# Kernel optimization log

Hardware: AMD Instinct MI355X
Metric: run time of the kernel (lower is better)

Reference implementation:

```python
import jax, jax.numpy as jnp
import numpy as np

NUM_NODES = 100_000
NUM_EDGES = 20_000
NNZ = 1_000_000


def setup_inputs() -> dict:
    key = jax.random.key(0)
    ks = jax.random.split(key, 8)
    d_in, d_hid, d_out = 128, 256, 40
    return {
        "x": jax.random.normal(ks[0], (NUM_NODES, d_in), dtype=jnp.float32),
        "node_idx": jax.random.randint(ks[1], (NNZ,), 0, NUM_NODES, dtype=jnp.int32),
        "edge_idx": jax.random.randint(ks[2], (NNZ,), 0, NUM_EDGES, dtype=jnp.int32),
        "W1": jax.random.normal(ks[3], (d_in, d_hid), dtype=jnp.float32) * (1.0 / np.sqrt(d_in)),
        "b1": jnp.zeros((d_hid,), dtype=jnp.float32),
        "W2": jax.random.normal(ks[4], (d_hid, d_hid), dtype=jnp.float32) * (1.0 / np.sqrt(d_hid)),
        "b2": jnp.zeros((d_hid,), dtype=jnp.float32),
        "W3": jax.random.normal(ks[5], (d_hid, d_out), dtype=jnp.float32) * (1.0 / np.sqrt(d_hid)),
        "b3": jnp.zeros((d_out,), dtype=jnp.float32),
    }


def _degree_norms(node_idx, edge_idx):
    # D = per-node incidence count (hyperedge_weight = ones); B = per-hyperedge node count
    ones = jnp.ones((node_idx.shape[0],), dtype=jnp.float32)
    D = jax.ops.segment_sum(ones, node_idx, num_segments=NUM_NODES)
    B = jax.ops.segment_sum(ones, edge_idx, num_segments=NUM_EDGES)
    Dinv = jnp.where(D > 0, 1.0 / D, 0.0)  # 1/D with inf -> 0, per PyG
    Binv = jnp.where(B > 0, 1.0 / B, 0.0)
    return Dinv, Binv


def _hconv(x, W, b, node_idx, edge_idx, Dinv, Binv):
    # PyG HypergraphConv (use_attention=False): X' = D^{-1} H B^{-1} H^T X W + b
    x = x @ W                                                            # [N, F]
    m = jax.ops.segment_sum(x[node_idx], edge_idx, num_segments=NUM_EDGES)  # H^T X W -> [E, F]
    m = Binv[:, None] * m
    out = jax.ops.segment_sum(m[edge_idx], node_idx, num_segments=NUM_NODES)  # [N, F]
    return Dinv[:, None] * out + b


def reference(x, node_idx, edge_idx, W1, b1, W2, b2, W3, b3):
    Dinv, Binv = _degree_norms(node_idx, edge_idx)
    # conv layers 0..L-2: conv -> ELU -> dropout (eval mode: identity)
    h = jax.nn.elu(_hconv(x, W1, b1, node_idx, edge_idx, Dinv, Binv))
    h = jax.nn.elu(_hconv(h, W2, b2, node_idx, edge_idx, Dinv, Binv))
    # final conv, no activation
    return _hconv(h, W3, b3, node_idx, edge_idx, Dinv, Binv)
```

## Files before the change

kernel.cpp:

```cpp
#include <hip/hip_runtime.h>
#include <cstdint>
#include <cstddef>

constexpr int N_NODES = 100000;
constexpr int N_EDGES = 20000;
constexpr int NNZ     = 1000000;
constexpr int NPAD    = 100096;
constexpr int EPAD    = 20096;

typedef __attribute__((ext_vector_type(8))) __bf16 bf16x8;
typedef __attribute__((ext_vector_type(4))) float f32x4;

__device__ __forceinline__ unsigned short bf16_rne(float v) {
  unsigned u = __builtin_bit_cast(unsigned, v);
  return (unsigned short)((u + 0x7FFFu + ((u >> 16) & 1u)) >> 16);
}
__device__ __forceinline__ void split2(float v, unsigned short& h, unsigned short& l) {
  unsigned u = __builtin_bit_cast(unsigned, v);
  unsigned hb = (u + 0x7FFFu + ((u >> 16) & 1u)) & 0xFFFF0000u;
  h = (unsigned short)(hb >> 16);
  float lo = v - __builtin_bit_cast(float, hb);
  l = bf16_rne(lo);
}
__device__ __forceinline__ float elu_f(float x) { return x > 0.f ? x : expm1f(x); }

__device__ __forceinline__ void gload_lds16(const void* g, void* l) {
  __builtin_amdgcn_global_load_lds(
      (const __attribute__((address_space(1))) unsigned int*)(uintptr_t)g,
      (__attribute__((address_space(3))) unsigned int*)(uintptr_t)l, 16, 0, 0);
}

__global__ void count_kernel(const int* __restrict__ ni, const int* __restrict__ ei,
                             int* __restrict__ dcnt, int* __restrict__ bcnt) {
  int i = blockIdx.x * blockDim.x + threadIdx.x;
  if (i < NNZ) {
    atomicAdd(&dcnt[ni[i]], 1);
    atomicAdd(&bcnt[ei[i]], 1);
  }
}

__global__ void invert2_kernel(const int* __restrict__ dcnt, const int* __restrict__ bcnt,
                               float* __restrict__ dinv, float* __restrict__ binv) {
  int i = blockIdx.x * blockDim.x + threadIdx.x;
  if (i < N_NODES) {
    int c = dcnt[i];
    dinv[i] = c > 0 ? 1.0f / (float)c : 0.0f;
  }
  if (i < N_EDGES) {
    int c = bcnt[i];
    binv[i] = c > 0 ? 1.0f / (float)c : 0.0f;
  }
}

__device__ __forceinline__ void scan_block_body(const int* __restrict__ cnt, int n,
                                                int* __restrict__ out,
                                                int* __restrict__ partials, int bid) {
  __shared__ int buf[256];
  int tid = threadIdx.x;
  int i = bid * 256 + tid;
  int v = (i < n) ? cnt[i] : 0;
  buf[tid] = v;
  __syncthreads();
  for (int o = 1; o < 256; o <<= 1) {
    int t = (tid >= o) ? buf[tid - o] : 0;
    __syncthreads();
    buf[tid] += t;
    __syncthreads();
  }
  if (i < n) out[i] = buf[tid] - v;
  if (tid == 255) partials[bid] = buf[tid];
}

__global__ void scan_block2(const int* __restrict__ c1, int n1, int* __restrict__ o1,
                            int* __restrict__ p1, int nb1,
                            const int* __restrict__ c2, int n2, int* __restrict__ o2,
                            int* __restrict__ p2) {
  if ((int)blockIdx.x < nb1) scan_block_body(c1, n1, o1, p1, blockIdx.x);
  else scan_block_body(c2, n2, o2, p2, blockIdx.x - nb1);
}

__device__ __forceinline__ void scan_partials_body(int* __restrict__ partials, int nb,
                                                   int* __restrict__ total_out) {
  __shared__ int buf[1024];
  int tid = threadIdx.x;
  int v = (tid < nb) ? partials[tid] : 0;
  buf[tid] = v;
  __syncthreads();
  for (int o = 1; o < 1024; o <<= 1) {
    int t = (tid >= o) ? buf[tid - o] : 0;
    __syncthreads();
    buf[tid] += t;
    __syncthreads();
  }
  if (tid < nb) partials[tid] = buf[tid] - v;
  if (tid == 1023) *total_out = buf[1023];
}

__global__ void scan_partials2(int* __restrict__ p1, int nb1, int* __restrict__ t1,
                               int* __restrict__ p2, int nb2, int* __restrict__ t2) {
  if (blockIdx.x == 0) scan_partials_body(p1, nb1, t1);
  else scan_partials_body(p2, nb2, t2);
}

__global__ void scan_add2(int* __restrict__ o1, int n1, const int* __restrict__ p1, int nb1,
                          int* __restrict__ o2, int n2, const int* __restrict__ p2) {
  if ((int)blockIdx.x < nb1) {
    int i = blockIdx.x * 256 + threadIdx.x;
    if (i < n1) o1[i] += p1[blockIdx.x];
  } else {
    int b = blockIdx.x - nb1;
    int i = b * 256 + threadIdx.x;
    if (i < n2) o2[i] += p2[b];
  }
}

__global__ void fill_kernel(const int* __restrict__ ni, const int* __restrict__ ei,
                            const int* __restrict__ noff, const int* __restrict__ eoff,
                            int* __restrict__ ncur, int* __restrict__ ecur,
                            int* __restrict__ nedges, int* __restrict__ enodes) {
  int i = blockIdx.x * blockDim.x + threadIdx.x;
  if (i < NNZ) {
    int n = ni[i], e = ei[i];
    int p = atomicAdd(&ecur[e], 1);
    enodes[eoff[e] + p] = n;
    int q = atomicAdd(&ncur[n], 1);
    nedges[noff[n] + q] = e;
  }
}

__global__ void wsplit_all(const float* __restrict__ W1, const float* __restrict__ W2,
                           const float* __restrict__ W3,
                           unsigned short* __restrict__ W1th, unsigned short* __restrict__ W1tl,
                           unsigned short* __restrict__ W2th, unsigned short* __restrict__ W2tl,
                           unsigned short* __restrict__ W3th, unsigned short* __restrict__ W3tl) {
  int i = blockIdx.x * 256 + threadIdx.x;
  float v;
  unsigned short h, l;
  if (i < 32768) {
    int n = i >> 7, k = i & 127;
    v = W1[(size_t)k * 256 + n];
    split2(v, h, l);
    W1th[i] = h; W1tl[i] = l;
  } else if (i < 98304) {
    int j = i - 32768;
    int n = j >> 8, k = j & 255;
    v = W2[(size_t)k * 256 + n];
    split2(v, h, l);
    W2th[j] = h; W2tl[j] = l;
  } else if (i < 110592) {
    int j = i - 98304;
    int n = j >> 8, k = j & 255;
    v = (n < 40) ? W3[(size_t)k * 40 + n] : 0.0f;
    split2(v, h, l);
    W3th[j] = h; W3tl[j] = l;
  }
}

template <int MFR, int NFR, int WAVES_M, int WAVES_N, int EPI>
__global__ __launch_bounds__(256) void gemm_tile(
    const unsigned short* __restrict__ Ah, const unsigned short* __restrict__ Al,
    const unsigned short* __restrict__ Bh, const unsigned short* __restrict__ Bl,
    int K, const float* __restrict__ bias, float* __restrict__ outF, int ncols,
    int Mrows) {
  constexpr int BM = WAVES_M * MFR * 16;
  constexpr int BN = WAVES_N * NFR * 16;
  __shared__ char lds[(BM + BN) * 128];
  char* Ash = lds;
  char* Asl = lds + BM * 64;
  char* Bsh = lds + BM * 128;
  char* Bsl = lds + BM * 128 + BN * 64;

  const int wave = threadIdx.x >> 6;
  const int lane = threadIdx.x & 63;
  const int rl = lane & 15;
  const int g = lane >> 4;
  const int wr = wave / WAVES_N;
  const int wc = wave % WAVES_N;
  const int rowbase = blockIdx.x * BM;
  const int colbase = blockIdx.y * BN;

  f32x4 acc[MFR][NFR] = {};

  auto stage = [&](const unsigned short* G, char* S, int R, int rbase, int k0) {
    for (int wi = wave; wi < (R >> 4); wi += 4) {
      int c = wi * 64 + lane;
      int row = c >> 2;
      int colbyte = ((lane & 3) * 16) ^ ((row & 3) << 4);
      const char* src = (const char*)G + ((size_t)(rbase + row) * K + k0) * 2 + colbyte;
      gload_lds16(src, S + wi * 1024);
    }
  };

  for (int k0 = 0; k0 < K; k0 += 32) {
    stage(Ah, Ash, BM, rowbase, k0);
    stage(Al, Asl, BM, rowbase, k0);
    stage(Bh, Bsh, BN, colbase, k0);
    stage(Bl, Bsl, BN, colbase, k0);
    asm volatile("s_waitcnt vmcnt(0)" ::: "memory");
    __syncthreads();

    bf16x8 afh[MFR], afl[MFR], bfh[NFR], bfl[NFR];
#pragma unroll
    for (int mf = 0; mf < MFR; ++mf) {
      int r = wr * MFR * 16 + mf * 16 + rl;
      int addr = r * 64 + ((g * 16) ^ ((r & 3) << 4));
      afh[mf] = *(const bf16x8*)(Ash + addr);
      afl[mf] = *(const bf16x8*)(Asl + addr);
    }
#pragma unroll
    for (int nf = 0; nf < NFR; ++nf) {
      int r = wc * NFR * 16 + nf * 16 + rl;
      int addr = r * 64 + ((g * 16) ^ ((r & 3) << 4));
      bfh[nf] = *(const bf16x8*)(Bsh + addr);
      bfl[nf] = *(const bf16x8*)(Bsl + addr);
    }
#pragma unroll
    for (int mf = 0; mf < MFR; ++mf)
#pragma unroll
      for (int nf = 0; nf < NFR; ++nf) {
        acc[mf][nf] = __builtin_amdgcn_mfma_f32_16x16x32_bf16(afh[mf], bfh[nf], acc[mf][nf], 0, 0, 0);
        acc[mf][nf] = __builtin_amdgcn_mfma_f32_16x16x32_bf16(afh[mf], bfl[nf], acc[mf][nf], 0, 0, 0);
        acc[mf][nf] = __builtin_amdgcn_mfma_f32_16x16x32_bf16(afl[mf], bfh[nf], acc[mf][nf], 0, 0, 0);
      }
    __syncthreads();
  }

#pragma unroll
  for (int mf = 0; mf < MFR; ++mf)
#pragma unroll
    for (int nf = 0; nf < NFR; ++nf)
#pragma unroll
      for (int i = 0; i < 4; ++i) {
        int grow = rowbase + wr * MFR * 16 + mf * 16 + g * 4 + i;
        if (grow >= Mrows) continue;
        int gcol = colbase + wc * NFR * 16 + nf * 16 + rl;
        if (gcol >= ncols) continue;
        float v = acc[mf][nf][i];
        if (EPI == 2) {
          v += bias[gcol];
          v = elu_f(v);
        }
        outF[(size_t)grow * ncols + gcol] = v;
      }
}

#define ACC4(a, v) { a.x += v.x; a.y += v.y; a.z += v.z; a.w += v.w; }

__global__ __launch_bounds__(256) void edge_reduce256_split(
    const float* __restrict__ h1, const int* __restrict__ eoff,
    const int* __restrict__ enodes, const float* __restrict__ binv,
    unsigned short* __restrict__ mh, unsigned short* __restrict__ ml) {
  int w = (blockIdx.x * blockDim.x + threadIdx.x) >> 6;
  int lane = threadIdx.x & 63;
  if (w >= EPAD) return;
  if (w >= N_EDGES) {
    uint2 z = {0, 0};
    *reinterpret_cast<uint2*>(&mh[(size_t)w * 256 + lane * 4]) = z;
    *reinterpret_cast<uint2*>(&ml[(size_t)w * 256 + lane * 4]) = z;
    return;
  }
  int s = eoff[w], t = eoff[w + 1];
  float4 a0 = {0, 0, 0, 0}, a1 = {0, 0, 0, 0}, a2 = {0, 0, 0, 0}, a3 = {0, 0, 0, 0};
  int j = s;
  for (; j < t && (j & 3); ++j) {
    float4 v = *reinterpret_cast<const float4*>(&h1[(size_t)enodes[j] * 256 + lane * 4]);
    ACC4(a0, v);
  }
  for (; j + 4 <= t; j += 4) {
    int4 idx = *reinterpret_cast<const int4*>(enodes + j);
    float4 v0 = *reinterpret_cast<const float4*>(&h1[(size_t)idx.x * 256 + lane * 4]);
    float4 v1 = *reinterpret_cast<const float4*>(&h1[(size_t)idx.y * 256 + lane * 4]);
    float4 v2 = *reinterpret_cast<const float4*>(&h1[(size_t)idx.z * 256 + lane * 4]);
    float4 v3 = *reinterpret_cast<const float4*>(&h1[(size_t)idx.w * 256 + lane * 4]);
    ACC4(a0, v0); ACC4(a1, v1); ACC4(a2, v2); ACC4(a3, v3);
  }
  for (; j < t; ++j) {
    float4 v = *reinterpret_cast<const float4*>(&h1[(size_t)enodes[j] * 256 + lane * 4]);
    ACC4(a0, v);
  }
  float bv = binv[w];
  float v0 = (a0.x + a1.x + a2.x + a3.x) * bv;
  float v1 = (a0.y + a1.y + a2.y + a3.y) * bv;
  float v2 = (a0.z + a1.z + a2.z + a3.z) * bv;
  float v3 = (a0.w + a1.w + a2.w + a3.w) * bv;
  unsigned short h0, l0, h1s, l1, h2, l2, h3, l3;
  split2(v0, h0, l0);
  split2(v1, h1s, l1);
  split2(v2, h2, l2);
  split2(v3, h3, l3);
  uint2 ph, pl;
  ph.x = (unsigned)h0 | ((unsigned)h1s << 16);
  ph.y = (unsigned)h2 | ((unsigned)h3 << 16);
  pl.x = (unsigned)l0 | ((unsigned)l1 << 16);
  pl.y = (unsigned)l2 | ((unsigned)l3 << 16);
  *reinterpret_cast<uint2*>(&mh[(size_t)w * 256 + lane * 4]) = ph;
  *reinterpret_cast<uint2*>(&ml[(size_t)w * 256 + lane * 4]) = pl;
}

__global__ __launch_bounds__(256) void node_reduce256_split_elu(
    const float* __restrict__ m, const int* __restrict__ noff,
    const int* __restrict__ nedges, const float* __restrict__ dinv,
    const float* __restrict__ bias, unsigned short* __restrict__ Ah,
    unsigned short* __restrict__ Al) {
  int w = (blockIdx.x * blockDim.x + threadIdx.x) >> 6;
  int lane = threadIdx.x & 63;
  if (w >= N_NODES) return;
  int s = noff[w], t = noff[w + 1];
  float4 a0 = {0, 0, 0, 0}, a1 = {0, 0, 0, 0}, a2 = {0, 0, 0, 0}, a3 = {0, 0, 0, 0};
  int j = s;
  for (; j < t && (j & 3); ++j) {
    float4 v = *reinterpret_cast<const float4*>(&m[(size_t)nedges[j] * 256 + lane * 4]);
    ACC4(a0, v);
  }
  for (; j + 4 <= t; j += 4) {
    int4 idx = *reinterpret_cast<const int4*>(nedges + j);
    float4 v0 = *reinterpret_cast<const float4*>(&m[(size_t)idx.x * 256 + lane * 4]);
    float4 v1 = *reinterpret_cast<const float4*>(&m[(size_t)idx.y * 256 + lane * 4]);
    float4 v2 = *reinterpret_cast<const float4*>(&m[(size_t)idx.z * 256 + lane * 4]);
    float4 v3 = *reinterpret_cast<const float4*>(&m[(size_t)idx.w * 256 + lane * 4]);
    ACC4(a0, v0); ACC4(a1, v1); ACC4(a2, v2); ACC4(a3, v3);
  }
  for (; j < t; ++j) {
    float4 v = *reinterpret_cast<const float4*>(&m[(size_t)nedges[j] * 256 + lane * 4]);
    ACC4(a0, v);
  }
  float dv = dinv[w];
  float4 b4 = *reinterpret_cast<const float4*>(&bias[lane * 4]);
  float v0 = elu_f((a0.x + a1.x + a2.x + a3.x) * dv + b4.x);
  float v1 = elu_f((a0.y + a1.y + a2.y + a3.y) * dv + b4.y);
  float v2 = elu_f((a0.z + a1.z + a2.z + a3.z) * dv + b4.z);
  float v3 = elu_f((a0.w + a1.w + a2.w + a3.w) * dv + b4.w);
  unsigned short h0, l0, h1, l1, h2, l2, h3, l3;
  split2(v0, h0, l0);
  split2(v1, h1, l1);
  split2(v2, h2, l2);
  split2(v3, h3, l3);
  uint2 ph, pl;
  ph.x = (unsigned)h0 | ((unsigned)h1 << 16);
  ph.y = (unsigned)h2 | ((unsigned)h3 << 16);
  pl.x = (unsigned)l0 | ((unsigned)l1 << 16);
  pl.y = (unsigned)l2 | ((unsigned)l3 << 16);
  *reinterpret_cast<uint2*>(&Ah[(size_t)w * 256 + lane * 4]) = ph;
  *reinterpret_cast<uint2*>(&Al[(size_t)w * 256 + lane * 4]) = pl;
}

__global__ __launch_bounds__(256) void edge_reduce128(const float* __restrict__ x,
                                                      const int* __restrict__ eoff,
                                                      const int* __restrict__ enodes,
                                                      const float* __restrict__ binv,
                                                      float* __restrict__ m) {
  int w = (blockIdx.x * blockDim.x + threadIdx.x) >> 6;
  int lane = threadIdx.x & 63;
  if (w >= N_EDGES) return;
  int s = eoff[w], t = eoff[w + 1];
  float2 a0 = {0, 0}, a1 = {0, 0}, a2 = {0, 0}, a3 = {0, 0};
  int j = s;
  for (; j < t && (j & 3); ++j) {
    float2 v = *reinterpret_cast<const float2*>(&x[(size_t)enodes[j] * 128 + lane * 2]);
    a0.x += v.x; a0.y += v.y;
  }
  for (; j + 4 <= t; j += 4) {
    int4 idx = *reinterpret_cast<const int4*>(enodes + j);
    float2 v0 = *reinterpret_cast<const float2*>(&x[(size_t)idx.x * 128 + lane * 2]);
    float2 v1 = *reinterpret_cast<const float2*>(&x[(size_t)idx.y * 128 + lane * 2]);
    float2 v2 = *reinterpret_cast<const float2*>(&x[(size_t)idx.z * 128 + lane * 2]);
    float2 v3 = *reinterpret_cast<const float2*>(&x[(size_t)idx.w * 128 + lane * 2]);
    a0.x += v0.x; a0.y += v0.y;
    a1.x += v1.x; a1.y += v1.y;
    a2.x += v2.x; a2.y += v2.y;
    a3.x += v3.x; a3.y += v3.y;
  }
  for (; j < t; ++j) {
    float2 v = *reinterpret_cast<const float2*>(&x[(size_t)enodes[j] * 128 + lane * 2]);
    a0.x += v.x; a0.y += v.y;
  }
  float bv = binv[w];
  float2 r;
  r.x = (a0.x + a1.x + a2.x + a3.x) * bv;
  r.y = (a0.y + a1.y + a2.y + a3.y) * bv;
  *reinterpret_cast<float2*>(&m[(size_t)w * 128 + lane * 2]) = r;
}

__global__ __launch_bounds__(256) void node_reduce128_split(const float* __restrict__ m,
                                                            const int* __restrict__ noff,
                                                            const int* __restrict__ nedges,
                                                            const float* __restrict__ dinv,
                                                            unsigned short* __restrict__ Ah,
                                                            unsigned short* __restrict__ Al) {
  int w = (blockIdx.x * blockDim.x + threadIdx.x) >> 6;
  int lane = threadIdx.x & 63;
  if (w >= N_NODES) return;
  int s = noff[w], t = noff[w + 1];
  float2 a0 = {0, 0}, a1 = {0, 0}, a2 = {0, 0}, a3 = {0, 0};
  int j = s;
  for (; j < t && (j & 3); ++j) {
    float2 v = *reinterpret_cast<const float2*>(&m[(size_t)nedges[j] * 128 + lane * 2]);
    a0.x += v.x; a0.y += v.y;
  }
  for (; j + 4 <= t; j += 4) {
    int4 idx = *reinterpret_cast<const int4*>(nedges + j);
    float2 v0 = *reinterpret_cast<const float2*>(&m[(size_t)idx.x * 128 + lane * 2]);
    float2 v1 = *reinterpret_cast<const float2*>(&m[(size_t)idx.y * 128 + lane * 2]);
    float2 v2 = *reinterpret_cast<const float2*>(&m[(size_t)idx.z * 128 + lane * 2]);
    float2 v3 = *reinterpret_cast<const float2*>(&m[(size_t)idx.w * 128 + lane * 2]);
    a0.x += v0.x; a0.y += v0.y;
    a1.x += v1.x; a1.y += v1.y;
    a2.x += v2.x; a2.y += v2.y;
    a3.x += v3.x; a3.y += v3.y;
  }
  for (; j < t; ++j) {
    float2 v = *reinterpret_cast<const float2*>(&m[(size_t)nedges[j] * 128 + lane * 2]);
    a0.x += v.x; a0.y += v.y;
  }
  float dv = dinv[w];
  float ax = (a0.x + a1.x + a2.x + a3.x) * dv;
  float ay = (a0.y + a1.y + a2.y + a3.y) * dv;
  unsigned short h0, l0, h1, l1;
  split2(ax, h0, l0);
  split2(ay, h1, l1);
  unsigned ph = (unsigned)h0 | ((unsigned)h1 << 16);
  unsigned pl = (unsigned)l0 | ((unsigned)l1 << 16);
  *reinterpret_cast<unsigned*>(&Ah[(size_t)w * 128 + lane * 2]) = ph;
  *reinterpret_cast<unsigned*>(&Al[(size_t)w * 128 + lane * 2]) = pl;
}

__global__ __launch_bounds__(256) void edge_reduce40(const float* __restrict__ xw,
                                                     const int* __restrict__ eoff,
                                                     const int* __restrict__ enodes,
                                                     const float* __restrict__ binv,
                                                     float* __restrict__ m) {
  int w = (blockIdx.x * blockDim.x + threadIdx.x) >> 6;
  int lane = threadIdx.x & 63;
  if (w >= N_EDGES || lane >= 40) return;
  int s = eoff[w], t = eoff[w + 1];
  float a0 = 0.f, a1 = 0.f, a2 = 0.f, a3 = 0.f;
  int j = s;
  for (; j < t && (j & 3); ++j) a0 += xw[(size_t)enodes[j] * 40 + lane];
  for (; j + 4 <= t; j += 4) {
    int4 idx = *reinterpret_cast<const int4*>(enodes + j);
    a0 += xw[(size_t)idx.x * 40 + lane];
    a1 += xw[(size_t)idx.y * 40 + lane];
    a2 += xw[(size_t)idx.z * 40 + lane];
    a3 += xw[(size_t)idx.w * 40 + lane];
  }
  for (; j < t; ++j) a0 += xw[(size_t)enodes[j] * 40 + lane];
  m[(size_t)w * 40 + lane] = (a0 + a1 + a2 + a3) * binv[w];
}

__global__ __launch_bounds__(256) void node_reduce40(const float* __restrict__ m,
                                                     const int* __restrict__ noff,
                                                     const int* __restrict__ nedges,
                                                     const float* __restrict__ dinv,
                                                     const float* __restrict__ bias,
                                                     float* __restrict__ out) {
  int w = (blockIdx.x * blockDim.x + threadIdx.x) >> 6;
  int lane = threadIdx.x & 63;
  if (w >= N_NODES || lane >= 40) return;
  int s = noff[w], t = noff[w + 1];
  float a0 = 0.f, a1 = 0.f, a2 = 0.f, a3 = 0.f;
  int j = s;
  for (; j < t && (j & 3); ++j) a0 += m[(size_t)nedges[j] * 40 + lane];
  for (; j + 4 <= t; j += 4) {
    int4 idx = *reinterpret_cast<const int4*>(nedges + j);
    a0 += m[(size_t)idx.x * 40 + lane];
    a1 += m[(size_t)idx.y * 40 + lane];
    a2 += m[(size_t)idx.z * 40 + lane];
    a3 += m[(size_t)idx.w * 40 + lane];
  }
  for (; j < t; ++j) a0 += m[(size_t)nedges[j] * 40 + lane];
  out[(size_t)w * 40 + lane] = (a0 + a1 + a2 + a3) * dinv[w] + bias[lane];
}

extern "C" void kernel_launch(void* const* d_in, const int* in_sizes, int n_in,
                              void* d_out, int out_size, void* d_ws, size_t ws_size,
                              hipStream_t stream) {
  const float* x  = (const float*)d_in[0];
  const int*   ni = (const int*)d_in[1];
  const int*   ei = (const int*)d_in[2];
  const float* W1 = (const float*)d_in[3];
  const float* b1 = (const float*)d_in[4];
  const float* W2 = (const float*)d_in[5];
  const float* b2 = (const float*)d_in[6];
  const float* W3 = (const float*)d_in[7];
  const float* b3 = (const float*)d_in[8];
  float* out = (float*)d_out;

  char* base = (char*)d_ws;
  size_t off = 0;
  auto take = [&](size_t bytes) -> char* {
    char* p = base + off;
    off += (bytes + 255) & ~(size_t)255;
    return p;
  };

  int* dcnt   = (int*)take((size_t)N_NODES * 4);
  int* bcnt   = (int*)take((size_t)N_EDGES * 4);
  int* ncur   = (int*)take((size_t)N_NODES * 4);
  int* ecur   = (int*)take((size_t)N_EDGES * 4);
  const size_t memset_span = 400128 + 80128 + 400128 + 80128;
  int* noff   = (int*)take((size_t)(N_NODES + 1) * 4);
  int* eoff   = (int*)take((size_t)(N_EDGES + 1) * 4);
  int* npart  = (int*)take((size_t)((N_NODES + 255) / 256) * 4);
  int* epart  = (int*)take((size_t)((N_EDGES + 255) / 256) * 4);
  int* nedges = (int*)take((size_t)NNZ * 4);
  int* enodes = (int*)take((size_t)NNZ * 4);
  float* dinv = (float*)take((size_t)N_NODES * 4);
  float* binv = (float*)take((size_t)N_EDGES * 4);

  unsigned short* W1th = (unsigned short*)take((size_t)256 * 128 * 2);
  unsigned short* W1tl = (unsigned short*)take((size_t)256 * 128 * 2);
  unsigned short* W2th = (unsigned short*)take((size_t)256 * 256 * 2);
  unsigned short* W2tl = (unsigned short*)take((size_t)256 * 256 * 2);
  unsigned short* W3th = (unsigned short*)take((size_t)48 * 256 * 2);
  unsigned short* W3tl = (unsigned short*)take((size_t)48 * 256 * 2);

  const size_t A2B = (size_t)NPAD * 256 * 2;
  char* R2 = take(2 * A2B);
  char* R3 = take(2 * A2B);

  float* h1 = (float*)R2;
  unsigned short* A3h = (unsigned short*)R2;
  unsigned short* A3l = (unsigned short*)(R2 + A2B);

  float* m128 = (float*)R3;
  unsigned short* A1h = (unsigned short*)(R3 + 10240000);
  unsigned short* A1l = (unsigned short*)(R3 + 10240000 + (size_t)NPAD * 128 * 2);

  const size_t MEB = (size_t)EPAD * 256 * 2;
  unsigned short* m2eh = (unsigned short*)R3;
  unsigned short* m2el = (unsigned short*)(R3 + MEB);
  float* m256f = (float*)(R3 + 2 * MEB);

  float* t3  = (float*)R3;
  float* m40 = (float*)(R3 + 16015360);

  hipMemsetAsync(dcnt, 0, memset_span, stream);
  count_kernel<<<(NNZ + 255) / 256, 256, 0, stream>>>(ni, ei, dcnt, bcnt);
  invert2_kernel<<<(N_NODES + 255) / 256, 256, 0, stream>>>(dcnt, bcnt, dinv, binv);

  const int nb_n = (N_NODES + 255) / 256;
  const int nb_e = (N_EDGES + 255) / 256;
  scan_block2<<<nb_n + nb_e, 256, 0, stream>>>(dcnt, N_NODES, noff, npart, nb_n,
                                               bcnt, N_EDGES, eoff, epart);
  scan_partials2<<<2, 1024, 0, stream>>>(npart, nb_n, &noff[N_NODES],
                                         epart, nb_e, &eoff[N_EDGES]);
  scan_add2<<<nb_n + nb_e, 256, 0, stream>>>(noff, N_NODES, npart, nb_n,
                                             eoff, N_EDGES, epart);
  fill_kernel<<<(NNZ + 255) / 256, 256, 0, stream>>>(ni, ei, noff, eoff, ncur, ecur, nedges, enodes);

  wsplit_all<<<(110592 + 255) / 256, 256, 0, stream>>>(W1, W2, W3, W1th, W1tl,
                                                       W2th, W2tl, W3th, W3tl);

  const int eblocks  = (N_EDGES * 64 + 255) / 256;
  const int epblocks = (EPAD * 64 + 255) / 256;
  const int nblocks  = (N_NODES * 64 + 255) / 256;
  const int gm  = NPAD / 128;
  const int gme = EPAD / 128;

  edge_reduce128<<<eblocks, 256, 0, stream>>>(x, eoff, enodes, binv, m128);
  node_reduce128_split<<<nblocks, 256, 0, stream>>>(m128, noff, nedges, dinv, A1h, A1l);
  gemm_tile<4, 4, 2, 2, 2><<<dim3(gm, 2), 256, 0, stream>>>(
      A1h, A1l, W1th, W1tl, 128, b1, h1, 256, N_NODES);

  edge_reduce256_split<<<epblocks, 256, 0, stream>>>(h1, eoff, enodes, binv, m2eh, m2el);
  gemm_tile<4, 4, 2, 2, 0><<<dim3(gme, 2), 256, 0, stream>>>(
      m2eh, m2el, W2th, W2tl, 256, nullptr, m256f, 256, N_EDGES);
  node_reduce256_split_elu<<<nblocks, 256, 0, stream>>>(m256f, noff, nedges, dinv, b2, A3h, A3l);

  gemm_tile<2, 3, 4, 1, 0><<<dim3(gm, 1), 256, 0, stream>>>(
      A3h, A3l, W3th, W3tl, 256, nullptr, t3, 40, N_NODES);
  edge_reduce40<<<eblocks, 256, 0, stream>>>(t3, eoff, enodes, binv, m40);
  node_reduce40<<<nblocks, 256, 0, stream>>>(m40, noff, nedges, dinv, b3, out);
}
```

Baseline: 812.9 us.

## Split node reductions into column passes and fuse setup kernels

The node-side gather reductions for the 128- and 256-wide features now run as several column passes of 64 scalar lanes each, grouped by block index. The intent is to shrink the working set of the gathered edge-message table per pass so it stays cache-resident. The degree count is merged with the weight split into one launch, and the inverse degrees are computed inside the scan kernel, which saves two launches. The cost is that the neighbor index lists are re-read once per pass and loads become scalar instead of vectorized.

```diff
diff --git a/kernel.cpp b/kernel.cpp
--- a/kernel.cpp
+++ b/kernel.cpp
@@ -30,35 +30,56 @@
       (__attribute__((address_space(3))) unsigned int*)(uintptr_t)l, 16, 0, 0);
 }
 
-__global__ void count_kernel(const int* __restrict__ ni, const int* __restrict__ ei,
-                             int* __restrict__ dcnt, int* __restrict__ bcnt) {
-  int i = blockIdx.x * blockDim.x + threadIdx.x;
-  if (i < NNZ) {
-    atomicAdd(&dcnt[ni[i]], 1);
-    atomicAdd(&bcnt[ei[i]], 1);
-  }
-}
-
-__global__ void invert2_kernel(const int* __restrict__ dcnt, const int* __restrict__ bcnt,
-                               float* __restrict__ dinv, float* __restrict__ binv) {
-  int i = blockIdx.x * blockDim.x + threadIdx.x;
-  if (i < N_NODES) {
-    int c = dcnt[i];
-    dinv[i] = c > 0 ? 1.0f / (float)c : 0.0f;
-  }
-  if (i < N_EDGES) {
-    int c = bcnt[i];
-    binv[i] = c > 0 ? 1.0f / (float)c : 0.0f;
+constexpr int COUNT_BLOCKS = (NNZ + 255) / 256;
+
+__global__ void count_wsplit(const int* __restrict__ ni, const int* __restrict__ ei,
+                             int* __restrict__ dcnt, int* __restrict__ bcnt,
+                             const float* __restrict__ W1, const float* __restrict__ W2,
+                             const float* __restrict__ W3,
+                             unsigned short* __restrict__ W1th, unsigned short* __restrict__ W1tl,
+                             unsigned short* __restrict__ W2th, unsigned short* __restrict__ W2tl,
+                             unsigned short* __restrict__ W3th, unsigned short* __restrict__ W3tl) {
+  int b = blockIdx.x;
+  if (b < COUNT_BLOCKS) {
+    int i = b * 256 + threadIdx.x;
+    if (i < NNZ) {
+      atomicAdd(&dcnt[ni[i]], 1);
+      atomicAdd(&bcnt[ei[i]], 1);
+    }
+  } else {
+    int i = (b - COUNT_BLOCKS) * 256 + threadIdx.x;
+    float v;
+    unsigned short h, l;
+    if (i < 32768) {
+      int n = i >> 7, k = i & 127;
+      v = W1[(size_t)k * 256 + n];
+      split2(v, h, l);
+      W1th[i] = h; W1tl[i] = l;
+    } else if (i < 98304) {
+      int j = i - 32768;
+      int n = j >> 8, k = j & 255;
+      v = W2[(size_t)k * 256 + n];
+      split2(v, h, l);
+      W2th[j] = h; W2tl[j] = l;
+    } else if (i < 110592) {
+      int j = i - 98304;
+      int n = j >> 8, k = j & 255;
+      v = (n < 40) ? W3[(size_t)k * 40 + n] : 0.0f;
+      split2(v, h, l);
+      W3th[j] = h; W3tl[j] = l;
+    }
   }
 }
 
 __device__ __forceinline__ void scan_block_body(const int* __restrict__ cnt, int n,
                                                 int* __restrict__ out,
-                                                int* __restrict__ partials, int bid) {
+                                                int* __restrict__ partials, int bid,
+                                                float* __restrict__ inv) {
   __shared__ int buf[256];
   int tid = threadIdx.x;
   int i = bid * 256 + tid;
   int v = (i < n) ? cnt[i] : 0;
+  if (i < n) inv[i] = v > 0 ? 1.0f / (float)v : 0.0f;
   buf[tid] = v;
   __syncthreads();
   for (int o = 1; o < 256; o <<= 1) {
@@ -74,9 +95,10 @@
 __global__ void scan_block2(const int* __restrict__ c1, int n1, int* __restrict__ o1,
                             int* __restrict__ p1, int nb1,
                             const int* __restrict__ c2, int n2, int* __restrict__ o2,
-                            int* __restrict__ p2) {
-  if ((int)blockIdx.x < nb1) scan_block_body(c1, n1, o1, p1, blockIdx.x);
-  else scan_block_body(c2, n2, o2, p2, blockIdx.x - nb1);
+                            int* __restrict__ p2,
+                            float* __restrict__ dinv, float* __restrict__ binv) {
+  if ((int)blockIdx.x < nb1) scan_block_body(c1, n1, o1, p1, blockIdx.x, dinv);
+  else scan_block_body(c2, n2, o2, p2, blockIdx.x - nb1, binv);
 }
 
 __device__ __forceinline__ void scan_partials_body(int* __restrict__ partials, int nb,
@@ -125,34 +147,6 @@
     enodes[eoff[e] + p] = n;
     int q = atomicAdd(&ncur[n], 1);
     nedges[noff[n] + q] = e;
-  }
-}
-
-__global__ void wsplit_all(const float* __restrict__ W1, const float* __restrict__ W2,
-                           const float* __restrict__ W3,
-                           unsigned short* __restrict__ W1th, unsigned short* __restrict__ W1tl,
-                           unsigned short* __restrict__ W2th, unsigned short* __restrict__ W2tl,
-                           unsigned short* __restrict__ W3th, unsigned short* __restrict__ W3tl) {
-  int i = blockIdx.x * 256 + threadIdx.x;
-  float v;
-  unsigned short h, l;
-  if (i < 32768) {
-    int n = i >> 7, k = i & 127;
-    v = W1[(size_t)k * 256 + n];
-    split2(v, h, l);
-    W1th[i] = h; W1tl[i] = l;
-  } else if (i < 98304) {
-    int j = i - 32768;
-    int n = j >> 8, k = j & 255;
-    v = W2[(size_t)k * 256 + n];
-    split2(v, h, l);
-    W2th[j] = h; W2tl[j] = l;
-  } else if (i < 110592) {
-    int j = i - 98304;
-    int n = j >> 8, k = j & 255;
-    v = (n < 40) ? W3[(size_t)k * 40 + n] : 0.0f;
-    split2(v, h, l);
-    W3th[j] = h; W3tl[j] = l;
   }
 }
 
@@ -297,51 +291,34 @@
   *reinterpret_cast<uint2*>(&ml[(size_t)w * 256 + lane * 4]) = pl;
 }
 
-__global__ __launch_bounds__(256) void node_reduce256_split_elu(
+__global__ __launch_bounds__(256) void node_reduce256_ps(
     const float* __restrict__ m, const int* __restrict__ noff,
     const int* __restrict__ nedges, const float* __restrict__ dinv,
     const float* __restrict__ bias, unsigned short* __restrict__ Ah,
     unsigned short* __restrict__ Al) {
-  int w = (blockIdx.x * blockDim.x + threadIdx.x) >> 6;
+  constexpr int BPP = N_NODES / 4;
+  int pass = blockIdx.x / BPP;
+  int blk  = blockIdx.x - pass * BPP;
+  int w = blk * 4 + (threadIdx.x >> 6);
   int lane = threadIdx.x & 63;
-  if (w >= N_NODES) return;
+  int col = pass * 64 + lane;
   int s = noff[w], t = noff[w + 1];
-  float4 a0 = {0, 0, 0, 0}, a1 = {0, 0, 0, 0}, a2 = {0, 0, 0, 0}, a3 = {0, 0, 0, 0};
+  float a0 = 0.f, a1 = 0.f, a2 = 0.f, a3 = 0.f;
   int j = s;
-  for (; j < t && (j & 3); ++j) {
-    float4 v = *reinterpret_cast<const float4*>(&m[(size_t)nedges[j] * 256 + lane * 4]);
-    ACC4(a0, v);
-  }
+  for (; j < t && (j & 3); ++j) a0 += m[(size_t)nedges[j] * 256 + col];
   for (; j + 4 <= t; j += 4) {
     int4 idx = *reinterpret_cast<const int4*>(nedges + j);
-    float4 v0 = *reinterpret_cast<const float4*>(&m[(size_t)idx.x * 256 + lane * 4]);
-    float4 v1 = *reinterpret_cast<const float4*>(&m[(size_t)idx.y * 256 + lane * 4]);
-    float4 v2 = *reinterpret_cast<const float4*>(&m[(size_t)idx.z * 256 + lane * 4]);
-    float4 v3 = *reinterpret_cast<const float4*>(&m[(size_t)idx.w * 256 + lane * 4]);
-    ACC4(a0, v0); ACC4(a1, v1); ACC4(a2, v2); ACC4(a3, v3);
-  }
-  for (; j < t; ++j) {
-    float4 v = *reinterpret_cast<const float4*>(&m[(size_t)nedges[j] * 256 + lane * 4]);
-    ACC4(a0, v);
-  }
-  float dv = dinv[w];
-  float4 b4 = *reinterpret_cast<const float4*>(&bias[lane * 4]);
-  float v0 = elu_f((a0.x + a1.x + a2.x + a3.x) * dv + b4.x);
-  float v1 = elu_f((a0.y + a1.y + a2.y + a3.y) * dv + b4.y);
-  float v2 = elu_f((a0.z + a1.z + a2.z + a3.z) * dv + b4.z);
-  float v3 = elu_f((a0.w + a1.w + a2.w + a3.w) * dv + b4.w);
-  unsigned short h0, l0, h1, l1, h2, l2, h3, l3;
-  split2(v0, h0, l0);
-  split2(v1, h1, l1);
-  split2(v2, h2, l2);
-  split2(v3, h3, l3);
-  uint2 ph, pl;
-  ph.x = (unsigned)h0 | ((unsigned)h1 << 16);
-  ph.y = (unsigned)h2 | ((unsigned)h3 << 16);
-  pl.x = (unsigned)l0 | ((unsigned)l1 << 16);
-  pl.y = (unsigned)l2 | ((unsigned)l3 << 16);
-  *reinterpret_cast<uint2*>(&Ah[(size_t)w * 256 + lane * 4]) = ph;
-  *reinterpret_cast<uint2*>(&Al[(size_t)w * 256 + lane * 4]) = pl;
+    a0 += m[(size_t)idx.x * 256 + col];
+    a1 += m[(size_t)idx.y * 256 + col];
+    a2 += m[(size_t)idx.z * 256 + col];
+    a3 += m[(size_t)idx.w * 256 + col];
+  }
+  for (; j < t; ++j) a0 += m[(size_t)nedges[j] * 256 + col];
+  float v = elu_f((a0 + a1 + a2 + a3) * dinv[w] + bias[col]);
+  unsigned short h, l;
+  split2(v, h, l);
+  Ah[(size_t)w * 256 + col] = h;
+  Al[(size_t)w * 256 + col] = l;
 }
 
 __global__ __launch_bounds__(256) void edge_reduce128(const float* __restrict__ x,
@@ -381,47 +358,33 @@
   *reinterpret_cast<float2*>(&m[(size_t)w * 128 + lane * 2]) = r;
 }
 
-__global__ __launch_bounds__(256) void node_reduce128_split(const float* __restrict__ m,
-                                                            const int* __restrict__ noff,
-                                                            const int* __restrict__ nedges,
-                                                            const float* __restrict__ dinv,
-                                                            unsigned short* __restrict__ Ah,
-                                                            unsigned short* __restrict__ Al) {
-  int w = (blockIdx.x * blockDim.x + threadIdx.x) >> 6;
+__global__ __launch_bounds__(256) void node_reduce128_ps(
+    const float* __restrict__ m, const int* __restrict__ noff,
+    const int* __restrict__ nedges, const float* __restrict__ dinv,
+    unsigned short* __restrict__ Ah, unsigned short* __restrict__ Al) {
+  constexpr int BPP = N_NODES / 4;
+  int pass = blockIdx.x / BPP;
+  int blk  = blockIdx.x - pass * BPP;
+  int w = blk * 4 + (threadIdx.x >> 6);
   int lane = threadIdx.x & 63;
-  if (w >= N_NODES) return;
+  int col = pass * 64 + lane;
   int s = noff[w], t = noff[w + 1];
-  float2 a0 = {0, 0}, a1 = {0, 0}, a2 = {0, 0}, a3 = {0, 0};
+  float a0 = 0.f, a1 = 0.f, a2 = 0.f, a3 = 0.f;
   int j = s;
-  for (; j < t && (j & 3); ++j) {
-    float2 v = *reinterpret_cast<const float2*>(&m[(size_t)nedges[j] * 128 + lane * 2]);
-    a0.x += v.x; a0.y += v.y;
-  }
+  for (; j < t && (j & 3); ++j) a0 += m[(size_t)nedges[j] * 128 + col];
   for (; j + 4 <= t; j += 4) {
     int4 idx = *reinterpret_cast<const int4*>(nedges + j);
-    float2 v0 = *reinterpret_cast<const float2*>(&m[(size_t)idx.x * 128 + lane * 2]);
-    float2 v1 = *reinterpret_cast<const float2*>(&m[(size_t)idx.y * 128 + lane * 2]);
-    float2 v2 = *reinterpret_cast<const float2*>(&m[(size_t)idx.z * 128 + lane * 2]);
-    float2 v3 = *reinterpret_cast<const float2*>(&m[(size_t)idx.w * 128 + lane * 2]);
-    a0.x += v0.x; a0.y += v0.y;
-    a1.x += v1.x; a1.y += v1.y;
-    a2.x += v2.x; a2.y += v2.y;
-    a3.x += v3.x; a3.y += v3.y;
-  }
-  for (; j < t; ++j) {
-    float2 v = *reinterpret_cast<const float2*>(&m[(size_t)nedges[j] * 128 + lane * 2]);
-    a0.x += v.x; a0.y += v.y;
-  }
-  float dv = dinv[w];
-  float ax = (a0.x + a1.x + a2.x + a3.x) * dv;
-  float ay = (a0.y + a1.y + a2.y + a3.y) * dv;
-  unsigned short h0, l0, h1, l1;
-  split2(ax, h0, l0);
-  split2(ay, h1, l1);
-  unsigned ph = (unsigned)h0 | ((unsigned)h1 << 16);
-  unsigned pl = (unsigned)l0 | ((unsigned)l1 << 16);
-  *reinterpret_cast<unsigned*>(&Ah[(size_t)w * 128 + lane * 2]) = ph;
-  *reinterpret_cast<unsigned*>(&Al[(size_t)w * 128 + lane * 2]) = pl;
+    a0 += m[(size_t)idx.x * 128 + col];
+    a1 += m[(size_t)idx.y * 128 + col];
+    a2 += m[(size_t)idx.z * 128 + col];
+    a3 += m[(size_t)idx.w * 128 + col];
+  }
+  for (; j < t; ++j) a0 += m[(size_t)nedges[j] * 128 + col];
+  float v = (a0 + a1 + a2 + a3) * dinv[w];
+  unsigned short h, l;
+  split2(v, h, l);
+  Ah[(size_t)w * 128 + col] = h;
+  Al[(size_t)w * 128 + col] = l;
 }
 
 __global__ __launch_bounds__(256) void edge_reduce40(const float* __restrict__ xw,
@@ -535,22 +498,19 @@
   float* m40 = (float*)(R3 + 16015360);
 
   hipMemsetAsync(dcnt, 0, memset_span, stream);
-  count_kernel<<<(NNZ + 255) / 256, 256, 0, stream>>>(ni, ei, dcnt, bcnt);
-  invert2_kernel<<<(N_NODES + 255) / 256, 256, 0, stream>>>(dcnt, bcnt, dinv, binv);
+  count_wsplit<<<COUNT_BLOCKS + (110592 + 255) / 256, 256, 0, stream>>>(
+      ni, ei, dcnt, bcnt, W1, W2, W3, W1th, W1tl, W2th, W2tl, W3th, W3tl);
 
   const int nb_n = (N_NODES + 255) / 256;
   const int nb_e = (N_EDGES + 255) / 256;
   scan_block2<<<nb_n + nb_e, 256, 0, stream>>>(dcnt, N_NODES, noff, npart, nb_n,
-                                               bcnt, N_EDGES, eoff, epart);
+                                               bcnt, N_EDGES, eoff, epart, dinv, binv);
   scan_partials2<<<2, 1024, 0, stream>>>(npart, nb_n, &noff[N_NODES],
                                          epart, nb_e, &eoff[N_EDGES]);
   scan_add2<<<nb_n + nb_e, 256, 0, stream>>>(noff, N_NODES, npart, nb_n,
                                              eoff, N_EDGES, epart);
   fill_kernel<<<(NNZ + 255) / 256, 256, 0, stream>>>(ni, ei, noff, eoff, ncur, ecur, nedges, enodes);
 
-  wsplit_all<<<(110592 + 255) / 256, 256, 0, stream>>>(W1, W2, W3, W1th, W1tl,
-                                                       W2th, W2tl, W3th, W3tl);
-
   const int eblocks  = (N_EDGES * 64 + 255) / 256;
   const int epblocks = (EPAD * 64 + 255) / 256;
   const int nblocks  = (N_NODES * 64 + 255) / 256;
@@ -558,14 +518,14 @@
   const int gme = EPAD / 128;
 
   edge_reduce128<<<eblocks, 256, 0, stream>>>(x, eoff, enodes, binv, m128);
-  node_reduce128_split<<<nblocks, 256, 0, stream>>>(m128, noff, nedges, dinv, A1h, A1l);
+  node_reduce128_ps<<<2 * (N_NODES / 4), 256, 0, stream>>>(m128, noff, nedges, dinv, A1h, A1l);
   gemm_tile<4, 4, 2, 2, 2><<<dim3(gm, 2), 256, 0, stream>>>(
       A1h, A1l, W1th, W1tl, 128, b1, h1, 256, N_NODES);
 
   edge_reduce256_split<<<epblocks, 256, 0, stream>>>(h1, eoff, enodes, binv, m2eh, m2el);
   gemm_tile<4, 4, 2, 2, 0><<<dim3(gme, 2), 256, 0, stream>>>(
       m2eh, m2el, W2th, W2tl, 256, nullptr, m256f, 256, N_EDGES);
-  node_reduce256_split_elu<<<nblocks, 256, 0, stream>>>(m256f, noff, nedges, dinv, b2, A3h, A3l);
+  node_reduce256_ps<<<4 * (N_NODES / 4), 256, 0, stream>>>(m256f, noff, nedges, dinv, b2, A3h, A3l);
 
   gemm_tile<2, 3, 4, 1, 0><<<dim3(gm, 1), 256, 0, stream>>>(
       A3h, A3l, W3th, W3tl, 256, nullptr, t3, 40, N_NODES);
```

Result: slower. 934.6 us (+15.0%).
